# Kernel tuning notes

Measured on AMD Instinct MI355X. Metric: run time of the kernel, lower is better.

Reference implementation:

```python
import jax, jax.numpy as jnp
import numpy as np

B, N, C, H, P = 8, 4096, 512, 8, 64
D = C // H


def setup_inputs() -> dict:
    key = jax.random.key(0)
    ks = jax.random.split(key, 5)
    s = 0.02
    return {
        "x": jax.random.normal(ks[0], (B, N, C), jnp.float32),
        "w_qkv": jax.random.normal(ks[1], (3 * C, C), jnp.float32) * s,
        "w_e": jax.random.normal(ks[2], (P, N), jnp.float32) * s,
        "b_e": jnp.zeros((P,), jnp.float32),
        "temperature": jnp.ones((1, 1, 1), jnp.float32),
        "temperature2": jnp.ones((H, 1, 1), jnp.float32),
        "w_o1": jax.random.normal(ks[3], (C // 2, C), jnp.float32) * s,
        "b_o1": jnp.zeros((C // 2,), jnp.float32),
        "w_o2": jax.random.normal(ks[4], (C // 2, C), jnp.float32) * s,
        "b_o2": jnp.zeros((C // 2,), jnp.float32),
    }


def reference(x, w_qkv, w_e, b_e, temperature, temperature2, w_o1, b_o1, w_o2, b_o2):
    Bs, Ns, Cs = x.shape
    # qkvv projection and head split: [B,N,3C] -> [3,B,H,N,D]
    qkv = (x @ w_qkv.T).reshape(Bs, Ns, 3, H, D)
    qkv = jnp.transpose(qkv, (2, 0, 3, 1, 4))
    q, k, v = qkv[0], qkv[1], qkv[2]
    q_t = jnp.swapaxes(q, -2, -1)  # [B,H,D,N]
    k_t = jnp.swapaxes(k, -2, -1)  # [B,H,D,N]
    v_t = jnp.swapaxes(v, -2, -1)  # [B,H,D,N]
    # Linformer-style projection along token axis; E = F (shared weights)
    kp = k_t @ w_e.T + b_e  # [B,H,D,P]
    vp = v_t @ w_e.T + b_e  # [B,H,D,P]
    # L2-normalize q along tokens (k is normalized in the original AFTER
    # projection, so that normalization is dead code and omitted)
    qn = q_t / jnp.maximum(jnp.linalg.norm(q_t, axis=-1, keepdims=True), 1e-12)
    # ---- channel attention: [B,C,C] scores over raw x ----
    xt = jnp.swapaxes(x, -2, -1)  # [B,C,N]
    attn_ca = jax.nn.softmax((xt @ x) * temperature, axis=-1)
    x_ca = jnp.swapaxes(attn_ca @ xt, -2, -1)  # [B,N,C]
    # ---- projected spatial attention: [B,H,N,P] scores ----
    attn_sa = jax.nn.softmax(
        jnp.einsum('bhdn,bhdp->bhnp', qn, kp) * temperature2, axis=-1)
    x_sa = jnp.einsum('bhnp,bhdp->bhnd', attn_sa, vp)  # [B,H,N,D]
    # faithful to torch: permute(0,3,1,2) then reshape(B,N,C)
    x_sa = jnp.transpose(x_sa, (0, 3, 1, 2)).reshape(Bs, Ns, Cs)
    out = jnp.concatenate(
        [x_sa @ w_o1.T + b_o1, x_ca @ w_o2.T + b_o2], axis=-1)
    return out
```

## Files before the change

kernel.cpp:

```cpp
#include <hip/hip_runtime.h>
#include <hip/hip_bf16.h>

typedef unsigned short u16;

#define AS1 __attribute__((address_space(1)))
#define AS3 __attribute__((address_space(3)))

static __device__ __forceinline__ float bl(u16 v) {
    return __uint_as_float(((unsigned)v) << 16);
}
static __device__ __forceinline__ u16 f2b(float f) {
    unsigned u = __float_as_uint(f);
    unsigned r = u + 0x7FFFu + ((u >> 16) & 1u);
    return (u16)(r >> 16);
}
static __device__ __forceinline__ float ldf(const void* p, long i, int isbf) {
    if (isbf) return bl(((const u16*)p)[i]);
    return ((const float*)p)[i];
}
static __device__ __forceinline__ void gload_lds16(const u16* g, u16* l) {
    __builtin_amdgcn_global_load_lds((const AS1 void*)g, (AS3 void*)l, 16, 0, 0);
}

typedef __attribute__((ext_vector_type(8))) short bf16x8;
typedef __attribute__((ext_vector_type(4))) float f32x4;

static __device__ __forceinline__ bf16x8 pack8(const float* p) {
    const float4 x0 = ((const float4*)p)[0];
    const float4 x1 = ((const float4*)p)[1];
    unsigned r0, r1, r2, r3;
    asm("v_cvt_pk_bf16_f32 %0, %1, %2" : "=v"(r0) : "v"(x0.x), "v"(x0.y));
    asm("v_cvt_pk_bf16_f32 %0, %1, %2" : "=v"(r1) : "v"(x0.z), "v"(x0.w));
    asm("v_cvt_pk_bf16_f32 %0, %1, %2" : "=v"(r2) : "v"(x1.x), "v"(x1.y));
    asm("v_cvt_pk_bf16_f32 %0, %1, %2" : "=v"(r3) : "v"(x1.z), "v"(x1.w));
    union { unsigned u[4]; bf16x8 v; } u;
    u.u[0] = r0; u.u[1] = r1; u.u[2] = r2; u.u[3] = r3;
    return u.v;
}

__global__ void dtype_probe(const void* __restrict__ temp, unsigned* __restrict__ flag) {
    if (threadIdx.x == 0 && blockIdx.x == 0)
        flag[0] = (((const u16*)temp)[0] == 0x3F80) ? 1u : 0u;
}

__global__ __launch_bounds__(256) void zero_f32(float* __restrict__ p, long n) {
    const long stride = (long)gridDim.x * 256;
    for (long i = (long)blockIdx.x * 256 + threadIdx.x; i < n; i += stride)
        p[i] = 0.f;
}

__global__ __launch_bounds__(256) void conv_x(const void* __restrict__ X,
                                              u16* __restrict__ xb,
                                              u16* __restrict__ xt,
                                              const unsigned* __restrict__ flg)
{
    __shared__ u16 tile[64][65];
    const int f = (int)flg[0];
    const int b = blockIdx.z;
    const int n0 = blockIdx.x * 64, c0 = blockIdx.y * 64;
    const int t = threadIdx.x, r0 = t >> 6, c = t & 63;
    #pragma unroll
    for (int rr = 0; rr < 16; ++rr) {
        const int r = rr * 4 + r0;
        const long gi = ((long)b * 4096 + n0 + r) * 512 + c0 + c;
        const u16 h = f2b(ldf(X, gi, f));
        xb[gi] = h;
        tile[r][c] = h;
    }
    __syncthreads();
    #pragma unroll
    for (int rr = 0; rr < 16; ++rr) {
        const int cc = rr * 4 + r0;
        xt[((long)b * 512 + c0 + cc) * 4096 + n0 + c] = tile[c][cc];
    }
}

__global__ __launch_bounds__(256) void conv_w(const void* __restrict__ W,
                                              u16* __restrict__ wb, long nelem,
                                              const unsigned* __restrict__ flg)
{
    const int f = (int)flg[0];
    const long stride = (long)gridDim.x * 256;
    for (long i = (long)blockIdx.x * 256 + threadIdx.x; i < nelem; i += stride)
        wb[i] = f2b(ldf(W, i, f));
}

__global__ __launch_bounds__(256) void gemm_mfma_nt(
    const u16* __restrict__ A, const u16* __restrict__ B,
    void* __restrict__ C, const void* __restrict__ bias,
    int M, int N, int K, int lda, int ldb, int ldc,
    long sA, long sB, long sC,
    const unsigned* __restrict__ flg, int biasExt, int cF32, int kSplit,
    float* __restrict__ qsq)
{
    __shared__ u16 Asm[2][128 * 32];
    __shared__ u16 Bsm[2][128 * 32];
    const int t = threadIdx.x, w = t >> 6, l = t & 63;
    const int gx = gridDim.x, gy = gridDim.y;
    const long nwg = (long)gx * gy * gridDim.z;
    const long lin = blockIdx.x + (long)gx * (blockIdx.y + (long)gy * blockIdx.z);
    long nid = lin;
    if ((nwg & 7) == 0) nid = (lin & 7) * (nwg >> 3) + (lin >> 3);
    const int by = (int)(nid % gy);
    const long r2 = nid / gy;
    const int bx = (int)(r2 % gx);
    int bz = (int)(r2 / gx), kz = 0;
    if (kSplit > 1) { kz = bz % kSplit; bz /= kSplit; }
    const u16* Ab = A + (long)bz * sA;
    const u16* Bb = B + (long)bz * sB;
    const int m0 = bx * 128, n0 = by * 128;
    const int wm = (w >> 1) * 64, wn = (w & 1) * 64;
    const int srow = l >> 2;
    const int scol = (l & 3) * 8;
    const int fr = l & 15;
    const int fk = (l >> 4) * 8;
    f32x4 acc[4][4];
    #pragma unroll
    for (int i = 0; i < 4; ++i)
        #pragma unroll
        for (int j = 0; j < 4; ++j)
            acc[i][j] = (f32x4){0.f, 0.f, 0.f, 0.f};

    const int kChunk = K / kSplit;
    const int kBeg = kz * kChunk, kEnd = kBeg + kChunk;
    const int q0 = w, q1 = w + 4;

#define STAGE(nb, kk)                                                                   \
    do {                                                                                \
        gload_lds16(Ab + (long)(m0 + q0 * 16 + srow) * lda + (kk) + scol, &Asm[nb][q0 * 512]); \
        gload_lds16(Ab + (long)(m0 + q1 * 16 + srow) * lda + (kk) + scol, &Asm[nb][q1 * 512]); \
        gload_lds16(Bb + (long)(n0 + q0 * 16 + srow) * ldb + (kk) + scol, &Bsm[nb][q0 * 512]); \
        gload_lds16(Bb + (long)(n0 + q1 * 16 + srow) * ldb + (kk) + scol, &Bsm[nb][q1 * 512]); \
    } while (0)

    STAGE(0, kBeg);
    __syncthreads();
    int cur = 0;
    for (int k0 = kBeg; k0 < kEnd; k0 += 32) {
        if (k0 + 32 < kEnd) STAGE(cur ^ 1, k0 + 32);
        bf16x8 af[4], bf[4];
        #pragma unroll
        for (int i = 0; i < 4; ++i) {
            af[i] = *(const bf16x8*)&Asm[cur][(wm + i * 16 + fr) * 32 + fk];
            bf[i] = *(const bf16x8*)&Bsm[cur][(wn + i * 16 + fr) * 32 + fk];
        }
        #pragma unroll
        for (int i = 0; i < 4; ++i)
            #pragma unroll
            for (int j = 0; j < 4; ++j)
                acc[i][j] = __builtin_amdgcn_mfma_f32_16x16x32_bf16(af[i], bf[j], acc[i][j], 0, 0, 0);
        __syncthreads();
        cur ^= 1;
    }
#undef STAGE

    const int f = (int)flg[0];
    const long cOff = (long)bz * sC;
    float bj[4] = {0.f, 0.f, 0.f, 0.f};
    if (bias) {
        #pragma unroll
        for (int j = 0; j < 4; ++j)
            bj[j] = ldf(bias, n0 + wn + j * 16 + fr, biasExt ? f : 1);
    }
    #pragma unroll
    for (int i = 0; i < 4; ++i) {
        #pragma unroll
        for (int j = 0; j < 4; ++j) {
            const int col = n0 + wn + j * 16 + fr;
            #pragma unroll
            for (int r = 0; r < 4; ++r) {
                const int row = m0 + wm + i * 16 + (l >> 4) * 4 + r;
                const float v = acc[i][j][r] + bj[j];
                if (kSplit > 1)
                    atomicAdd(&((float*)C)[cOff + (long)row * ldc + col], v);
                else if (cF32)
                    ((float*)C)[cOff + (long)row * ldc + col] = v;
                else
                    ((u16*)C)[cOff + (long)row * ldc + col] = f2b(v);
            }
        }
    }
    if (qsq) {
        #pragma unroll
        for (int j = 0; j < 4; ++j) {
            const int col = n0 + wn + j * 16 + fr;
            if (col < 512) {
                float s = 0.f;
                #pragma unroll
                for (int i = 0; i < 4; ++i)
                    #pragma unroll
                    for (int r = 0; r < 4; ++r)
                        s = fmaf(acc[i][j][r], acc[i][j][r], s);
                s += __shfl_xor(s, 16, 64);
                s += __shfl_xor(s, 32, 64);
                if ((l >> 4) == 0)
                    atomicAdd(&qsq[(long)bz * 512 + col], s);
            }
        }
    }
}

__global__ __launch_bounds__(256) void xe_mfma(const u16* __restrict__ WEB,
                                               const u16* __restrict__ XT,
                                               float* __restrict__ XE)
{
    const int t = threadIdx.x, w = t >> 6, l = t & 63;
    const int l15 = l & 15, g = l >> 4;
    const int c0 = blockIdx.x * 128 + (w >> 1) * 64;
    const int b = blockIdx.y;
    const int nbase = blockIdx.z * 512 + (w & 1) * 256;
    f32x4 acc[4][4];
    #pragma unroll
    for (int i = 0; i < 4; ++i)
        #pragma unroll
        for (int j = 0; j < 4; ++j)
            acc[i][j] = (f32x4){0.f, 0.f, 0.f, 0.f};
    for (int ks = 0; ks < 8; ++ks) {
        const int n = nbase + ks * 32 + g * 8;
        bf16x8 a[4], bb[4];
        #pragma unroll
        for (int i = 0; i < 4; ++i)
            a[i] = *(const bf16x8*)&WEB[(long)(i * 16 + l15) * 4096 + n];
        #pragma unroll
        for (int j = 0; j < 4; ++j)
            bb[j] = *(const bf16x8*)&XT[((long)b * 512 + c0 + j * 16 + l15) * 4096 + n];
        #pragma unroll
        for (int i = 0; i < 4; ++i)
            #pragma unroll
            for (int j = 0; j < 4; ++j)
                acc[i][j] = __builtin_amdgcn_mfma_f32_16x16x32_bf16(a[i], bb[j], acc[i][j], 0, 0, 0);
    }
    #pragma unroll
    for (int i = 0; i < 4; ++i)
        #pragma unroll
        for (int j = 0; j < 4; ++j)
            #pragma unroll
            for (int r = 0; r < 4; ++r)
                atomicAdd(&XE[((long)b * 64 + i * 16 + g * 4 + r) * 512 + c0 + j * 16 + l15],
                          acc[i][j][r]);
}

__global__ __launch_bounds__(256) void kpvp2_mfma(const float* __restrict__ XE,
                                                  const u16* __restrict__ WQB,
                                                  const float* __restrict__ qsq,
                                                  const void* __restrict__ be,
                                                  const void* __restrict__ temp2,
                                                  u16* __restrict__ kpT,
                                                  u16* __restrict__ vpB,
                                                  const unsigned* __restrict__ flg)
{
    __shared__ float lds[4][4096];
    const int bh = blockIdx.x, b = bh >> 3, h = bh & 7;
    const int t = threadIdx.x, w = t >> 6, l = t & 63;
    const int l15 = l & 15, g = l >> 4;
    const int isV = w >> 1;
    const int ch = w & 1;
    const u16* wrow = WQB + (long)(512 + isV * 512 + h * 64) * 512;
    const float* xr = XE + (long)b * 64 * 512;
    f32x4 acc[4][4];
    #pragma unroll
    for (int i = 0; i < 4; ++i)
        #pragma unroll
        for (int j = 0; j < 4; ++j)
            acc[i][j] = (f32x4){0.f, 0.f, 0.f, 0.f};
    for (int ks = 0; ks < 8; ++ks) {
        const int c = ch * 256 + ks * 32 + g * 8;
        bf16x8 a[4], bb[4];
        if (!isV) {
            #pragma unroll
            for (int i = 0; i < 4; ++i)
                a[i] = pack8(&xr[(long)(i * 16 + l15) * 512 + c]);
            #pragma unroll
            for (int j = 0; j < 4; ++j)
                bb[j] = *(const bf16x8*)&wrow[(long)(j * 16 + l15) * 512 + c];
        } else {
            #pragma unroll
            for (int i = 0; i < 4; ++i)
                a[i] = *(const bf16x8*)&wrow[(long)(i * 16 + l15) * 512 + c];
            #pragma unroll
            for (int j = 0; j < 4; ++j)
                bb[j] = pack8(&xr[(long)(j * 16 + l15) * 512 + c]);
        }
        #pragma unroll
        for (int i = 0; i < 4; ++i)
            #pragma unroll
            for (int j = 0; j < 4; ++j)
                acc[i][j] = __builtin_amdgcn_mfma_f32_16x16x32_bf16(a[i], bb[j], acc[i][j], 0, 0, 0);
    }
    #pragma unroll
    for (int i = 0; i < 4; ++i)
        #pragma unroll
        for (int j = 0; j < 4; ++j)
            #pragma unroll
            for (int r = 0; r < 4; ++r)
                lds[w][(i * 16 + g * 4 + r) * 64 + j * 16 + l15] = acc[i][j][r];
    __syncthreads();
    const int f = (int)flg[0];
    if (t < 128) {
        const float t2 = ldf(temp2, h, f);
        for (int e = t; e < 4096; e += 128) {
            const int p = e >> 6, d = e & 63;
            const float rn = 1.0f / fmaxf(sqrtf(qsq[b * 512 + h * 64 + d]), 1e-12f);
            kpT[(long)bh * 4096 + e] = f2b((lds[0][e] + lds[1][e] + ldf(be, p, f)) * rn * t2);
        }
    } else {
        for (int e = t - 128; e < 4096; e += 128) {
            vpB[(long)bh * 4096 + e] = f2b(lds[2][e] + lds[3][e] + ldf(be, e & 63, f));
        }
    }
}

__global__ __launch_bounds__(256) void softmax_ca(const float* __restrict__ S,
                                                  u16* __restrict__ A,
                                                  const void* __restrict__ temp,
                                                  const unsigned* __restrict__ flg)
{
    __shared__ float red[256];
    const int row = blockIdx.x;
    const int t = threadIdx.x;
    const float tv = ldf(temp, 0, (int)flg[0]);
    const float* s = S + (long)row * 512;
    float v0 = s[t] * tv;
    float v1 = s[t + 256] * tv;
    red[t] = fmaxf(v0, v1);
    __syncthreads();
    for (int o = 128; o > 0; o >>= 1) {
        if (t < o) red[t] = fmaxf(red[t], red[t + o]);
        __syncthreads();
    }
    const float m = red[0];
    __syncthreads();
    float e0 = expf(v0 - m), e1 = expf(v1 - m);
    red[t] = e0 + e1;
    __syncthreads();
    for (int o = 128; o > 0; o >>= 1) {
        if (t < o) red[t] += red[t + o];
        __syncthreads();
    }
    const float inv = 1.0f / red[0];
    u16* a = A + (long)row * 512;
    a[t]       = f2b(e0 * inv);
    a[t + 256] = f2b(e1 * inv);
}

__global__ __launch_bounds__(256) void spatial_attn_mfma(
    const u16* __restrict__ Q, const u16* __restrict__ kpT,
    const u16* __restrict__ vpB, u16* __restrict__ XSA)
{
    __shared__ u16 P[4][4096];
    const int bh = blockIdx.y, b = bh >> 3, h = bh & 7;
    const int t = threadIdx.x, w = t >> 6, l = t & 63;
    const int l15 = l & 15, g = l >> 4;
    const int n0 = blockIdx.x * 256 + w * 64;
    char* Pw = (char*)&P[w][0];

    const u16* kb = kpT + (long)bh * 4096;
    const u16* vb = vpB + (long)bh * 4096;
    bf16x8 akp[2][4], avp[2][4];
    #pragma unroll
    for (int ks = 0; ks < 2; ++ks)
        #pragma unroll
        for (int i = 0; i < 4; ++i) {
            akp[ks][i] = *(const bf16x8*)&kb[(i * 16 + l15) * 64 + ks * 32 + g * 8];
            avp[ks][i] = *(const bf16x8*)&vb[(i * 16 + l15) * 64 + ks * 32 + g * 8];
        }

    f32x4 sacc[4][4];
    #pragma unroll
    for (int i = 0; i < 4; ++i)
        #pragma unroll
        for (int j = 0; j < 4; ++j)
            sacc[i][j] = (f32x4){0.f, 0.f, 0.f, 0.f};
    const u16* qb = Q + ((long)b * 4096 + n0) * 512 + h * 64;
    #pragma unroll
    for (int ks = 0; ks < 2; ++ks) {
        bf16x8 bq[4];
        #pragma unroll
        for (int j = 0; j < 4; ++j)
            bq[j] = *(const bf16x8*)&qb[(long)(j * 16 + l15) * 512 + ks * 32 + g * 8];
        #pragma unroll
        for (int i = 0; i < 4; ++i)
            #pragma unroll
            for (int j = 0; j < 4; ++j)
                sacc[i][j] = __builtin_amdgcn_mfma_f32_16x16x32_bf16(akp[ks][i], bq[j], sacc[i][j], 0, 0, 0);
    }

    #pragma unroll
    for (int j = 0; j < 4; ++j) {
        float m = sacc[0][j][0];
        #pragma unroll
        for (int i = 0; i < 4; ++i)
            #pragma unroll
            for (int r = 0; r < 4; ++r)
                m = fmaxf(m, sacc[i][j][r]);
        m = fmaxf(m, __shfl_xor(m, 16, 64));
        m = fmaxf(m, __shfl_xor(m, 32, 64));
        float s = 0.f;
        #pragma unroll
        for (int i = 0; i < 4; ++i)
            #pragma unroll
            for (int r = 0; r < 4; ++r) {
                const float e = __expf(sacc[i][j][r] - m);
                sacc[i][j][r] = e;
                s += e;
            }
        s += __shfl_xor(s, 16, 64);
        s += __shfl_xor(s, 32, 64);
        const float inv = 1.0f / s;
        const int n = j * 16 + l15;
        const int swz = (n & 7) << 4;
        #pragma unroll
        for (int i = 0; i < 4; ++i) {
            unsigned lo, hi;
            float p0 = sacc[i][j][0] * inv, p1 = sacc[i][j][1] * inv;
            float p2 = sacc[i][j][2] * inv, p3 = sacc[i][j][3] * inv;
            asm("v_cvt_pk_bf16_f32 %0, %1, %2" : "=v"(lo) : "v"(p0), "v"(p1));
            asm("v_cvt_pk_bf16_f32 %0, %1, %2" : "=v"(hi) : "v"(p2), "v"(p3));
            const int byte = (n * 128 + i * 32 + g * 8) ^ swz;
            *(uint2*)(Pw + byte) = make_uint2(lo, hi);
        }
    }

    f32x4 oacc[4][4];
    #pragma unroll
    for (int i = 0; i < 4; ++i)
        #pragma unroll
        for (int j = 0; j < 4; ++j)
            oacc[i][j] = (f32x4){0.f, 0.f, 0.f, 0.f};
    #pragma unroll
    for (int ks = 0; ks < 2; ++ks) {
        bf16x8 bp[4];
        #pragma unroll
        for (int j = 0; j < 4; ++j) {
            const int n = j * 16 + l15;
            const int byte = (n * 128 + ks * 64 + g * 16) ^ ((n & 7) << 4);
            bp[j] = *(const bf16x8*)(Pw + byte);
        }
        #pragma unroll
        for (int i = 0; i < 4; ++i)
            #pragma unroll
            for (int j = 0; j < 4; ++j)
                oacc[i][j] = __builtin_amdgcn_mfma_f32_16x16x32_bf16(avp[ks][i], bp[j], oacc[i][j], 0, 0, 0);
    }

    const int rowoff = h * 8 + (n0 >> 9);
    const int colbase = n0 & 511;
    #pragma unroll
    for (int i = 0; i < 4; ++i)
        #pragma unroll
        for (int r = 0; r < 4; ++r) {
            const int d = i * 16 + g * 4 + r;
            u16* orow = XSA + ((long)b * 4096 + d * 64 + rowoff) * 512 + colbase;
            #pragma unroll
            for (int j = 0; j < 4; ++j)
                orow[j * 16 + l15] = f2b(oacc[i][j][r]);
        }
}

extern "C" void kernel_launch(void* const* d_in, const int* in_sizes, int n_in,
                              void* d_out, int out_size, void* d_ws, size_t ws_size,
                              hipStream_t stream)
{
    const void* x     = d_in[0];
    const void* w_qkv = d_in[1];
    const void* w_e   = d_in[2];
    const void* b_e   = d_in[3];
    const void* temp  = d_in[4];
    const void* temp2 = d_in[5];
    const void* w_o1  = d_in[6];
    const void* b_o1  = d_in[7];
    const void* w_o2  = d_in[8];
    const void* b_o2  = d_in[9];
    float* out = (float*)d_out;

    char* ws = (char*)d_ws;
    unsigned* flag = (unsigned*)ws; ws += 256;
    u16*   qb     = (u16*)ws;   ws += (size_t)8 * 4096 * 512 * 2;
    float* qsq    = (float*)ws; ws += (size_t)4096 * 4;
    float* xe     = (float*)ws; ws += (size_t)8 * 64 * 512 * 4;
    float* scores = (float*)ws; ws += (size_t)8 * 512 * 512 * 4;
    u16*   attn   = (u16*)ws;   ws += (size_t)8 * 512 * 512 * 2;
    u16*   x_ca   = (u16*)ws;   ws += (size_t)8 * 4096 * 512 * 2;
    u16*   xt     = (u16*)ws;   ws += (size_t)8 * 512 * 4096 * 2;
    u16*   xb     = (u16*)ws;   ws += (size_t)8 * 4096 * 512 * 2;
    u16*   wqb    = (u16*)ws;   ws += (size_t)1536 * 512 * 2;
    u16*   web    = (u16*)ws;   ws += (size_t)64 * 4096 * 2;
    u16*   wo1b   = (u16*)ws;   ws += (size_t)256 * 512 * 2;
    u16*   wo2b   = (u16*)ws;   ws += (size_t)256 * 512 * 2;
    u16*   kpT    = (u16*)ws;   ws += (size_t)262144 * 2;
    u16*   vpB    = (u16*)ws;   ws += (size_t)262144 * 2;
    u16*   x_sa   = xt;

    dtype_probe<<<1, 64, 0, stream>>>(temp, flag);
    conv_x<<<dim3(64, 8, 8), 256, 0, stream>>>(x, xb, xt, flag);
    conv_w<<<768, 256, 0, stream>>>(w_qkv, wqb, 1536L * 512, flag);
    conv_w<<<128, 256, 0, stream>>>(w_e, web, 64L * 4096, flag);
    conv_w<<<128, 256, 0, stream>>>(w_o1, wo1b, 256L * 512, flag);
    conv_w<<<128, 256, 0, stream>>>(w_o2, wo2b, 256L * 512, flag);
    zero_f32<<<4, 256, 0, stream>>>(qsq, 4096);
    gemm_mfma_nt<<<dim3(32, 4, 8), 256, 0, stream>>>(
        xb, wqb, qb, nullptr, 4096, 512, 512, 512, 512, 512,
        (long)4096 * 512, 0, (long)4096 * 512, flag, 0, 0, 1, qsq);
    zero_f32<<<128, 256, 0, stream>>>(xe, (long)8 * 64 * 512);
    xe_mfma<<<dim3(4, 8, 8), 256, 0, stream>>>(web, xt, xe);
    kpvp2_mfma<<<64, 256, 0, stream>>>(xe, wqb, qsq, b_e, temp2, kpT, vpB, flag);
    zero_f32<<<2048, 256, 0, stream>>>(scores, (long)8 * 512 * 512);
    gemm_mfma_nt<<<dim3(4, 4, 32), 256, 0, stream>>>(
        xt, xt, scores, nullptr, 512, 512, 4096, 4096, 4096, 512,
        (long)512 * 4096, (long)512 * 4096, (long)512 * 512, flag, 0, 1, 4, nullptr);
    softmax_ca<<<4096, 256, 0, stream>>>(scores, attn, temp, flag);
    gemm_mfma_nt<<<dim3(32, 4, 8), 256, 0, stream>>>(
        xb, attn, x_ca, nullptr, 4096, 512, 512, 512, 512, 512,
        (long)4096 * 512, (long)512 * 512, (long)4096 * 512, flag, 0, 0, 1, nullptr);
    spatial_attn_mfma<<<dim3(16, 64), 256, 0, stream>>>(qb, kpT, vpB, x_sa);
    gemm_mfma_nt<<<dim3(32, 2, 8), 256, 0, stream>>>(
        x_sa, wo1b, out, b_o1, 4096, 256, 512, 512, 512, 512,
        (long)4096 * 512, 0, (long)4096 * 512, flag, 1, 1, 1, nullptr);
    gemm_mfma_nt<<<dim3(32, 2, 8), 256, 0, stream>>>(
        x_ca, wo2b, out + 256, b_o2, 4096, 256, 512, 512, 512, 512,
        (long)4096 * 512, 0, (long)4096 * 512, flag, 1, 1, 1, nullptr);
}
```

Measured before the change: 398.9 us.

## Add 256x256-tile 512-thread GEMM kernel and fuse the two output projections

Adds a new GEMM kernel with 256x256 output tiles, 8 waves, XOR-swizzled LDS, double buffering and an XCD-aware block remap. It replaces the Q projection, the channel-attention apply GEMM and both output projections. The two output GEMMs are merged into one launch that picks operands by column block. Larger tiles raise data reuse and cut launches, but the grid shrinks to 256 workgroups and each thread holds more registers, which may leave CUs underused.

```diff
diff --git a/kernel.cpp b/kernel.cpp
--- a/kernel.cpp
+++ b/kernel.cpp
@@ -200,6 +200,121 @@
     }
 }
 
+__global__ __launch_bounds__(512, 2) void gemm256_nt(
+    const u16* __restrict__ A, const u16* __restrict__ B,
+    void* __restrict__ C, const void* __restrict__ bias,
+    int K, int lda, int ldb, int ldc,
+    long sA, long sB, long sC,
+    const unsigned* __restrict__ flg, int biasExt, int cF32,
+    float* __restrict__ qsq,
+    const u16* __restrict__ A2, const u16* __restrict__ B2,
+    const void* __restrict__ bias2, int nSwitch)
+{
+    __shared__ u16 Asm[2][256 * 32];
+    __shared__ u16 Bsm[2][256 * 32];
+    const int t = threadIdx.x, w = t >> 6, l = t & 63;
+    const int gx = gridDim.x, gy = gridDim.y;
+    const long nwg = (long)gx * gy * gridDim.z;
+    const long lin = blockIdx.x + (long)gx * (blockIdx.y + (long)gy * blockIdx.z);
+    long nid = lin;
+    if ((nwg & 7) == 0) nid = (lin & 7) * (nwg >> 3) + (lin >> 3);
+    const int by = (int)(nid % gy);
+    const long r2 = nid / gy;
+    const int bx = (int)(r2 % gx);
+    const int bz = (int)(r2 / gx);
+    const int m0 = bx * 256, n0 = by * 256;
+    const u16* Asel = A; const u16* Bsel = B; const void* bsel = bias;
+    int nLoc = n0;
+    if (A2 && n0 >= nSwitch) { Asel = A2; Bsel = B2; bsel = bias2; nLoc = n0 - nSwitch; }
+    const u16* Ab = Asel + (long)bz * sA;
+    const u16* Bb = Bsel + (long)bz * sB + (long)nLoc * ldb;
+    const int wm = (w >> 1) * 64, wn = (w & 1) * 128;
+    const int srow = l >> 2;
+    const int selem = (((l & 3) ^ (srow & 3)) << 3);
+    const int fr = l & 15;
+    const int fk = (l >> 4) * 8;
+    const int xorv = (fr & 3) << 3;
+    f32x4 acc[4][8];
+    #pragma unroll
+    for (int i = 0; i < 4; ++i)
+        #pragma unroll
+        for (int j = 0; j < 8; ++j)
+            acc[i][j] = (f32x4){0.f, 0.f, 0.f, 0.f};
+
+#define STAGE256(nb, kk)                                                                     \
+    do {                                                                                     \
+        gload_lds16(Ab + (long)(m0 + w * 16 + srow) * lda + (kk) + selem, &Asm[nb][w * 512]);        \
+        gload_lds16(Ab + (long)(m0 + (w + 8) * 16 + srow) * lda + (kk) + selem, &Asm[nb][(w + 8) * 512]); \
+        gload_lds16(Bb + (long)(w * 16 + srow) * ldb + (kk) + selem, &Bsm[nb][w * 512]);             \
+        gload_lds16(Bb + (long)((w + 8) * 16 + srow) * ldb + (kk) + selem, &Bsm[nb][(w + 8) * 512]);     \
+    } while (0)
+
+    STAGE256(0, 0);
+    __syncthreads();
+    int cur = 0;
+    for (int k0 = 0; k0 < K; k0 += 32) {
+        if (k0 + 32 < K) STAGE256(cur ^ 1, k0 + 32);
+        bf16x8 af[4], bf[8];
+        #pragma unroll
+        for (int i = 0; i < 4; ++i)
+            af[i] = *(const bf16x8*)&Asm[cur][((wm + i * 16 + fr) << 5) + (fk ^ xorv)];
+        #pragma unroll
+        for (int j = 0; j < 8; ++j)
+            bf[j] = *(const bf16x8*)&Bsm[cur][((wn + j * 16 + fr) << 5) + (fk ^ xorv)];
+        #pragma unroll
+        for (int i = 0; i < 4; ++i)
+            #pragma unroll
+            for (int j = 0; j < 8; ++j)
+                acc[i][j] = __builtin_amdgcn_mfma_f32_16x16x32_bf16(af[i], bf[j], acc[i][j], 0, 0, 0);
+        __syncthreads();
+        cur ^= 1;
+    }
+#undef STAGE256
+
+    const int f = (int)flg[0];
+    const long cOff = (long)bz * sC;
+    float bj[8];
+    #pragma unroll
+    for (int j = 0; j < 8; ++j) bj[j] = 0.f;
+    if (bsel) {
+        #pragma unroll
+        for (int j = 0; j < 8; ++j)
+            bj[j] = ldf(bsel, (nLoc & 255) + wn + j * 16 + fr, biasExt ? f : 1);
+    }
+    #pragma unroll
+    for (int i = 0; i < 4; ++i) {
+        #pragma unroll
+        for (int j = 0; j < 8; ++j) {
+            const int col = n0 + wn + j * 16 + fr;
+            #pragma unroll
+            for (int r = 0; r < 4; ++r) {
+                const int row = m0 + wm + i * 16 + (l >> 4) * 4 + r;
+                const float v = acc[i][j][r] + bj[j];
+                if (cF32) ((float*)C)[cOff + (long)row * ldc + col] = v;
+                else      ((u16*)C)[cOff + (long)row * ldc + col] = f2b(v);
+            }
+        }
+    }
+    if (qsq) {
+        #pragma unroll
+        for (int j = 0; j < 8; ++j) {
+            const int col = n0 + wn + j * 16 + fr;
+            if (col < 512) {
+                float s = 0.f;
+                #pragma unroll
+                for (int i = 0; i < 4; ++i)
+                    #pragma unroll
+                    for (int r = 0; r < 4; ++r)
+                        s = fmaf(acc[i][j][r], acc[i][j][r], s);
+                s += __shfl_xor(s, 16, 64);
+                s += __shfl_xor(s, 32, 64);
+                if ((l >> 4) == 0)
+                    atomicAdd(&qsq[(long)bz * 512 + col], s);
+            }
+        }
+    }
+}
+
 __global__ __launch_bounds__(256) void xe_mfma(const u16* __restrict__ WEB,
                                                const u16* __restrict__ XT,
                                                float* __restrict__ XE)
@@ -498,9 +613,10 @@
     conv_w<<<128, 256, 0, stream>>>(w_o1, wo1b, 256L * 512, flag);
     conv_w<<<128, 256, 0, stream>>>(w_o2, wo2b, 256L * 512, flag);
     zero_f32<<<4, 256, 0, stream>>>(qsq, 4096);
-    gemm_mfma_nt<<<dim3(32, 4, 8), 256, 0, stream>>>(
-        xb, wqb, qb, nullptr, 4096, 512, 512, 512, 512, 512,
-        (long)4096 * 512, 0, (long)4096 * 512, flag, 0, 0, 1, qsq);
+    gemm256_nt<<<dim3(16, 2, 8), 512, 0, stream>>>(
+        xb, wqb, qb, nullptr, 512, 512, 512, 512,
+        (long)4096 * 512, 0, (long)4096 * 512, flag, 0, 0, qsq,
+        nullptr, nullptr, nullptr, 1 << 30);
     zero_f32<<<128, 256, 0, stream>>>(xe, (long)8 * 64 * 512);
     xe_mfma<<<dim3(4, 8, 8), 256, 0, stream>>>(web, xt, xe);
     kpvp2_mfma<<<64, 256, 0, stream>>>(xe, wqb, qsq, b_e, temp2, kpT, vpB, flag);
@@ -509,14 +625,13 @@
         xt, xt, scores, nullptr, 512, 512, 4096, 4096, 4096, 512,
         (long)512 * 4096, (long)512 * 4096, (long)512 * 512, flag, 0, 1, 4, nullptr);
     softmax_ca<<<4096, 256, 0, stream>>>(scores, attn, temp, flag);
-    gemm_mfma_nt<<<dim3(32, 4, 8), 256, 0, stream>>>(
-        xb, attn, x_ca, nullptr, 4096, 512, 512, 512, 512, 512,
-        (long)4096 * 512, (long)512 * 512, (long)4096 * 512, flag, 0, 0, 1, nullptr);
+    gemm256_nt<<<dim3(16, 2, 8), 512, 0, stream>>>(
+        xb, attn, x_ca, nullptr, 512, 512, 512, 512,
+        (long)4096 * 512, (long)512 * 512, (long)4096 * 512, flag, 0, 0, nullptr,
+        nullptr, nullptr, nullptr, 1 << 30);
     spatial_attn_mfma<<<dim3(16, 64), 256, 0, stream>>>(qb, kpT, vpB, x_sa);
-    gemm_mfma_nt<<<dim3(32, 2, 8), 256, 0, stream>>>(
-        x_sa, wo1b, out, b_o1, 4096, 256, 512, 512, 512, 512,
-        (long)4096 * 512, 0, (long)4096 * 512, flag, 1, 1, 1, nullptr);
-    gemm_mfma_nt<<<dim3(32, 2, 8), 256, 0, stream>>>(
-        x_ca, wo2b, out + 256, b_o2, 4096, 256, 512, 512, 512, 512,
-        (long)4096 * 512, 0, (long)4096 * 512, flag, 1, 1, 1, nullptr);
-}
+    gemm256_nt<<<dim3(16, 2, 8), 512, 0, stream>>>(
+        x_sa, wo1b, out, b_o1, 512, 512, 512, 512,
+        (long)4096 * 512, 0, (long)4096 * 512, flag, 1, 1, nullptr,
+        x_ca, wo2b, b_o2, 256);
+}
```

Result: faster. 378.4 us (-5.1%).
